# Performance work log

Hardware: AMD Instinct MI355X
Metric: run time of the kernel (lower is better)

The kernel has to match this reference:

```python
import jax, jax.numpy as jnp
import numpy as np

SCALE = 0.125  # quantization scale applied inline in the custom matmul
PAD = 4
STRIDE = 1


def setup_inputs() -> dict:
    key = jax.random.key(0)
    k1, k2, k3 = jax.random.split(key, 3)
    x = jax.random.normal(k1, (8, 64, 16384), dtype=jnp.float32)        # (N, C, L)
    weight = jax.random.normal(k2, (64, 64, 9), dtype=jnp.float32) * 0.05  # (O, I, K)
    bias = jax.random.normal(k3, (64,), dtype=jnp.float32)               # (O,)
    return {"x": x, "weight": weight, "bias": bias}


def reference(x, weight, bias):
    # Mathematically identical to: im2col unfold -> (N, out_l, C*K) @ (C*K, O),
    # then out * scale + bias. Expressed as a fused conv to avoid the huge
    # intermediate while computing the same result.
    out = jax.lax.conv_general_dilated(
        x, weight,
        window_strides=(STRIDE,),
        padding=[(PAD, PAD)],
        dimension_numbers=("NCH", "OIH", "NCH"),
    )  # (N, O, out_l)
    return out * SCALE + bias[None, :, None]
```

## Files before the change

kernel.cpp:

```cpp
#include <hip/hip_runtime.h>
#include <hip/hip_bf16.h>

#define C_IN    64
#define L_IN    16384
#define O_OUT   64
#define KTAP    9
#define LTILE   256
#define ROWS    272
#define RSTRIDE 72

typedef short          bf16x8 __attribute__((ext_vector_type(8)));
typedef unsigned short u16x8  __attribute__((ext_vector_type(8)));
typedef unsigned int   u32x4  __attribute__((ext_vector_type(4)));
typedef float          f32x4  __attribute__((ext_vector_type(4)));
typedef float          f32x8v __attribute__((ext_vector_type(8)));

static __device__ __forceinline__ unsigned short f2bf(float f) {
  __hip_bfloat16 h = __float2bfloat16(f);
  return __builtin_bit_cast(unsigned short, h);
}

static __device__ __forceinline__ unsigned int pk2(float lo, float hi) {
  return (unsigned int)f2bf(lo) | ((unsigned int)f2bf(hi) << 16);
}

__global__ void w_rearrange(const float* __restrict__ w,
                            unsigned short* __restrict__ w2) {
    int i = blockIdx.x * 256 + threadIdx.x;
    if (i >= KTAP * O_OUT * C_IN) return;
    int t  = i >> 12;
    int oc = i & 4095;
    w2[i] = f2bf(w[oc * KTAP + t] * 0.125f);
}

__global__ __launch_bounds__(256) void qconv_kernel(
    const float* __restrict__ x,
    const unsigned short* __restrict__ w2,
    const float* __restrict__ bias,
    float* __restrict__ out) {

  __shared__ __align__(16) unsigned short xs[ROWS][RSTRIDE];

  const int tid = threadIdx.x;
  const int n   = blockIdx.x >> 6;
  const int l0  = (blockIdx.x & 63) << 8;
  const float* xn = x + (size_t)n * C_IN * L_IN;

  for (int idx = tid; idx < ROWS; idx += 256) {
    const int cb = idx & 7;
    const int lb = idx >> 3;
    const int c0 = cb << 3;
    const int gl0 = l0 - 8 + (lb << 3);
    if (gl0 >= 0 && gl0 + 8 <= L_IN) {
      f32x8v v[8];
#pragma unroll
      for (int i = 0; i < 8; ++i)
        v[i] = *reinterpret_cast<const f32x8v*>(xn + (size_t)(c0 + i) * L_IN + gl0);
#pragma unroll
      for (int j = 0; j < 8; ++j) {
        u32x4 wv;
#pragma unroll
        for (int p = 0; p < 4; ++p)
          wv[p] = pk2(v[2 * p][j], v[2 * p + 1][j]);
        *reinterpret_cast<u32x4*>(&xs[(lb << 3) + j][c0]) = wv;
      }
    } else {
      unsigned short vb[8][8];
      for (int i = 0; i < 8; ++i)
        for (int j = 0; j < 8; ++j) {
          int gl = gl0 + j;
          vb[i][j] = (gl >= 0 && gl < L_IN)
                         ? f2bf(xn[(size_t)(c0 + i) * L_IN + gl])
                         : (unsigned short)0;
        }
      for (int j = 0; j < 8; ++j) {
        u16x8 wv;
        for (int i = 0; i < 8; ++i) wv[i] = vb[i][j];
        *reinterpret_cast<u16x8*>(&xs[(lb << 3) + j][c0]) = wv;
      }
    }
  }
  __syncthreads();

  const int wave = tid >> 6;
  const int lane = tid & 63;
  const int wr   = wave >> 1;
  const int wc   = wave & 1;
  const int col  = lane & 15;
  const int quad = lane >> 4;

  f32x4 acc[2][8];
#pragma unroll
  for (int m = 0; m < 2; ++m)
#pragma unroll
    for (int lt = 0; lt < 8; ++lt) acc[m][lt] = (f32x4){0.f, 0.f, 0.f, 0.f};

  const int rbase = (wc << 7) + col + 4;

  for (int t = 0; t < KTAP; ++t) {
    bf16x8 a[2][2];
#pragma unroll
    for (int m = 0; m < 2; ++m)
#pragma unroll
      for (int k = 0; k < 2; ++k)
        a[m][k] = *reinterpret_cast<const bf16x8*>(
            w2 + (t << 12) + (((wr << 5) + (m << 4) + col) << 6) + (k << 5) + (quad << 3));

#pragma unroll
    for (int k = 0; k < 2; ++k) {
#pragma unroll
      for (int lt = 0; lt < 8; ++lt) {
        const int r = rbase + t + (lt << 4);
        const bf16x8 b = *reinterpret_cast<const bf16x8*>(&xs[r][(k << 5) + (quad << 3)]);
        acc[0][lt] = __builtin_amdgcn_mfma_f32_16x16x32_bf16(a[0][k], b, acc[0][lt], 0, 0, 0);
        acc[1][lt] = __builtin_amdgcn_mfma_f32_16x16x32_bf16(a[1][k], b, acc[1][lt], 0, 0, 0);
      }
    }
  }

#pragma unroll
  for (int m = 0; m < 2; ++m) {
    const int obase = (wr << 5) + (m << 4) + (quad << 2);
    float bv[4];
#pragma unroll
    for (int reg = 0; reg < 4; ++reg) bv[reg] = bias[obase + reg];
#pragma unroll
    for (int lt = 0; lt < 8; ++lt) {
      const int l = l0 + (wc << 7) + (lt << 4) + col;
#pragma unroll
      for (int reg = 0; reg < 4; ++reg) {
        const int o = obase + reg;
        out[((size_t)(n * O_OUT + o) << 14) + l] = acc[m][lt][reg] + bv[reg];
      }
    }
  }
}

extern "C" void kernel_launch(void* const* d_in, const int* in_sizes, int n_in,
                              void* d_out, int out_size, void* d_ws, size_t ws_size,
                              hipStream_t stream) {
  const float*    x    = (const float*)d_in[0];
  const float*    w    = (const float*)d_in[1];
  const float*    bias = (const float*)d_in[2];
  float*          out  = (float*)d_out;
  unsigned short* w2   = (unsigned short*)d_ws;

  w_rearrange<<<(KTAP * O_OUT * C_IN + 255) / 256, 256, 0, stream>>>(w, w2);

  qconv_kernel<<<8 * (L_IN / LTILE), 256, 0, stream>>>(x, w2, bias, out);
}
```

Before: 97.93 us.

## Pre-transpose input to padded bf16 channels-last buffer in separate kernel

Adds an x_transpose kernel that converts x to bf16 and writes it channels-last into a workspace buffer, with zero halo rows at each sequence end. The conv kernel then fills shared memory with plain 16-byte copies, dropping the in-kernel conversion and the boundary branch. This costs an extra launch and a full write plus re-read of a 16 MB intermediate, against fp32 input reads totalling 32 MB.

```diff
diff --git a/kernel.cpp b/kernel.cpp
--- a/kernel.cpp
+++ b/kernel.cpp
@@ -8,9 +8,10 @@
 #define LTILE   256
 #define ROWS    272
 #define RSTRIDE 72
+#define XT_ROWS (L_IN + 16)
+#define XT_OFF  131072
 
 typedef short          bf16x8 __attribute__((ext_vector_type(8)));
-typedef unsigned short u16x8  __attribute__((ext_vector_type(8)));
 typedef unsigned int   u32x4  __attribute__((ext_vector_type(4)));
 typedef float          f32x4  __attribute__((ext_vector_type(4)));
 typedef float          f32x8v __attribute__((ext_vector_type(8)));
@@ -19,7 +20,6 @@
   __hip_bfloat16 h = __float2bfloat16(f);
   return __builtin_bit_cast(unsigned short, h);
 }
-
 static __device__ __forceinline__ unsigned int pk2(float lo, float hi) {
   return (unsigned int)f2bf(lo) | ((unsigned int)f2bf(hi) << 16);
 }
@@ -33,8 +33,53 @@
     w2[i] = f2bf(w[oc * KTAP + t] * 0.125f);
 }
 
+__global__ __launch_bounds__(256) void x_transpose(
+    const float* __restrict__ x, unsigned short* __restrict__ xt) {
+  __shared__ __align__(16) unsigned short xs[LTILE][RSTRIDE];
+  const int tid = threadIdx.x;
+  const int n   = blockIdx.x >> 6;
+  const int l0  = (blockIdx.x & 63) << 8;
+  const float* xn = x + (size_t)n * C_IN * L_IN;
+  unsigned short* xtn = xt + (size_t)n * XT_ROWS * C_IN;
+
+  {
+    const int lb = tid >> 3, cb = tid & 7;
+    const int c0 = cb << 3, gl0 = l0 + (lb << 3);
+    f32x8v v[8];
+#pragma unroll
+    for (int i = 0; i < 8; ++i)
+      v[i] = *reinterpret_cast<const f32x8v*>(xn + (size_t)(c0 + i) * L_IN + gl0);
+#pragma unroll
+    for (int j = 0; j < 8; ++j) {
+      u32x4 wv;
+#pragma unroll
+      for (int p = 0; p < 4; ++p) wv[p] = pk2(v[2 * p][j], v[2 * p + 1][j]);
+      *reinterpret_cast<u32x4*>(&xs[(lb << 3) + j][c0]) = wv;
+    }
+  }
+  __syncthreads();
+
+#pragma unroll
+  for (int it = 0; it < 8; ++it) {
+    const int idx = tid + (it << 8);
+    const int row = idx >> 3, ci = (idx & 7) << 3;
+    u32x4 wv = *reinterpret_cast<const u32x4*>(&xs[row][ci]);
+    *reinterpret_cast<u32x4*>(xtn + (size_t)(8 + l0 + row) * C_IN + ci) = wv;
+  }
+  if (l0 == 0 && tid < 64) {
+    const int row = tid >> 3, ci = (tid & 7) << 3;
+    u32x4 z = (u32x4){0u, 0u, 0u, 0u};
+    *reinterpret_cast<u32x4*>(xtn + (size_t)row * C_IN + ci) = z;
+  }
+  if (l0 == (L_IN - LTILE) && tid < 64) {
+    const int row = (L_IN + 8) + (tid >> 3), ci = (tid & 7) << 3;
+    u32x4 z = (u32x4){0u, 0u, 0u, 0u};
+    *reinterpret_cast<u32x4*>(xtn + (size_t)row * C_IN + ci) = z;
+  }
+}
+
 __global__ __launch_bounds__(256) void qconv_kernel(
-    const float* __restrict__ x,
+    const unsigned short* __restrict__ xt,
     const unsigned short* __restrict__ w2,
     const float* __restrict__ bias,
     float* __restrict__ out) {
@@ -44,40 +89,15 @@
   const int tid = threadIdx.x;
   const int n   = blockIdx.x >> 6;
   const int l0  = (blockIdx.x & 63) << 8;
-  const float* xn = x + (size_t)n * C_IN * L_IN;
+  const unsigned short* src = xt + ((size_t)n * XT_ROWS + l0) * C_IN;
 
-  for (int idx = tid; idx < ROWS; idx += 256) {
-    const int cb = idx & 7;
-    const int lb = idx >> 3;
-    const int c0 = cb << 3;
-    const int gl0 = l0 - 8 + (lb << 3);
-    if (gl0 >= 0 && gl0 + 8 <= L_IN) {
-      f32x8v v[8];
 #pragma unroll
-      for (int i = 0; i < 8; ++i)
-        v[i] = *reinterpret_cast<const f32x8v*>(xn + (size_t)(c0 + i) * L_IN + gl0);
-#pragma unroll
-      for (int j = 0; j < 8; ++j) {
-        u32x4 wv;
-#pragma unroll
-        for (int p = 0; p < 4; ++p)
-          wv[p] = pk2(v[2 * p][j], v[2 * p + 1][j]);
-        *reinterpret_cast<u32x4*>(&xs[(lb << 3) + j][c0]) = wv;
-      }
-    } else {
-      unsigned short vb[8][8];
-      for (int i = 0; i < 8; ++i)
-        for (int j = 0; j < 8; ++j) {
-          int gl = gl0 + j;
-          vb[i][j] = (gl >= 0 && gl < L_IN)
-                         ? f2bf(xn[(size_t)(c0 + i) * L_IN + gl])
-                         : (unsigned short)0;
-        }
-      for (int j = 0; j < 8; ++j) {
-        u16x8 wv;
-        for (int i = 0; i < 8; ++i) wv[i] = vb[i][j];
-        *reinterpret_cast<u16x8*>(&xs[(lb << 3) + j][c0]) = wv;
-      }
+  for (int it = 0; it < 9; ++it) {
+    const int idx = tid + (it << 8);
+    if (idx < ROWS * 8) {
+      const int row = idx >> 3, ci = (idx & 7) << 3;
+      u32x4 v = *reinterpret_cast<const u32x4*>(src + (size_t)row * C_IN + ci);
+      *reinterpret_cast<u32x4*>(&xs[row][ci]) = v;
     }
   }
   __syncthreads();
@@ -144,8 +164,9 @@
   const float*    bias = (const float*)d_in[2];
   float*          out  = (float*)d_out;
   unsigned short* w2   = (unsigned short*)d_ws;
+  unsigned short* xt   = (unsigned short*)((char*)d_ws + XT_OFF);
 
   w_rearrange<<<(KTAP * O_OUT * C_IN + 255) / 256, 256, 0, stream>>>(w, w2);
-
-  qconv_kernel<<<8 * (L_IN / LTILE), 256, 0, stream>>>(x, w2, bias, out);
+  x_transpose<<<8 * (L_IN / LTILE), 256, 0, stream>>>(x, xt);
+  qconv_kernel<<<8 * (L_IN / LTILE), 256, 0, stream>>>(xt, w2, bias, out);
 }
```

Result: slower. 104.7 us (+6.9%).
